# Optimization experiments

Measured on AMD Instinct MI355X. Metric: run time of the kernel, lower is better.

## Reference

```python
import jax, jax.numpy as jnp
import numpy as np

# Fixed problem sizes (equal-sized batch segments, matching setup_inputs)
B, N, M = 4, 4096, 16384          # clouds, coarse pts/cloud, fine pts/cloud
C_IN, C_SKIP, K = 256, 256, 3     # feature dims, knn k
CH = [C_IN + C_SKIP, 512, 256]    # MLP channels
EPS = 1e-16


def setup_inputs() -> dict:
    key = jax.random.key(0)
    ks = jax.random.split(key, 6)
    x = jax.random.normal(ks[0], (B * N, C_IN), jnp.float32)
    pos = jax.random.uniform(ks[1], (B * N, 3), jnp.float32)
    batch = jnp.repeat(jnp.arange(B, dtype=jnp.int64), N)
    x_skip = jax.random.normal(ks[2], (B * M, C_SKIP), jnp.float32)
    pos_skip = jax.random.uniform(ks[3], (B * M, 3), jnp.float32)
    batch_skip = jnp.repeat(jnp.arange(B, dtype=jnp.int64), M)
    W1 = jax.random.normal(ks[4], (CH[0], CH[1]), jnp.float32) / np.sqrt(CH[0]).astype(np.float32)
    b1 = jnp.zeros((CH[1],), jnp.float32)
    W2 = jax.random.normal(ks[5], (CH[1], CH[2]), jnp.float32) / np.sqrt(CH[1]).astype(np.float32)
    b2 = jnp.zeros((CH[2],), jnp.float32)
    return dict(x=x, pos=pos, batch=batch, x_skip=x_skip, pos_skip=pos_skip,
                batch_skip=batch_skip, W1=W1, b1=b1, W2=W2, b2=b2)


def _knn_interpolate(x, pos, pos_skip):
    """torch_geometric.nn.knn_interpolate with equal-sized batch segments."""
    xb = x.reshape(B, N, C_IN)
    ps = pos.reshape(B, N, 3)
    qs = pos_skip.reshape(B, M, 3)
    # squared pairwise distances [B, M, N]
    d2 = (jnp.sum(qs * qs, -1)[:, :, None]
          - 2.0 * jnp.einsum('bmd,bnd->bmn', qs, ps)
          + jnp.sum(ps * ps, -1)[:, None, :])
    neg_d2, idx = jax.lax.top_k(-d2, K)                # k smallest distances, [B,M,K]
    w = 1.0 / jnp.clip(-neg_d2, EPS)                   # inverse squared distance weights
    feats = jax.vmap(lambda f, i: f[i])(xb, idx)       # gather: [B, M, K, C_IN]
    y = jnp.sum(w[..., None] * feats, axis=2) / jnp.sum(w, axis=2)[..., None]
    return y.reshape(B * M, C_IN)


def reference(x, pos, batch, x_skip, pos_skip, batch_skip, W1, b1, W2, b2):
    y = _knn_interpolate(x, pos, pos_skip)
    h = jnp.concatenate([y, x_skip], axis=1)           # [B*M, 512]
    h = jax.nn.relu(h @ W1 + b1)
    h = jax.nn.relu(h @ W2 + b2)
    return h, pos_skip, batch_skip
```

## Files before the change

kernel.cpp:

```cpp
#include <hip/hip_runtime.h>
#include <stdint.h>

#define NB 4
#define NPTS 4096
#define MPTS 16384
#define CIN 256
#define CH0 512
#define CH1 512
#define CH2 256
#define ROWS (NB * MPTS)
#define POS_OUT_OFF (ROWS * CH2)
#define BATCH_OUT_OFF (POS_OUT_OFF + ROWS * 3)
#define CELL_CAP 40
#define QCAP 96

using u16 = unsigned short;
using u32 = unsigned int;
using u64 = unsigned long long;

typedef __bf16 bf16x8 __attribute__((ext_vector_type(8)));
typedef float f32x4 __attribute__((ext_vector_type(4)));

__device__ __forceinline__ u16 f2bf(float f) {
  u32 u = __builtin_bit_cast(u32, f);
  u32 r = u + 0x7fffu + ((u >> 16) & 1u);
  return (u16)(r >> 16);
}

__device__ __forceinline__ u32 flipf(float f) {
  u32 u = __builtin_bit_cast(u32, f);
  return u ^ ((u32)((int)u >> 31) | 0x80000000u);
}
__device__ __forceinline__ float unflipf(u32 f) {
  u32 m = (~(u32)((int)f >> 31)) | 0x80000000u;
  return __builtin_bit_cast(float, f ^ m);
}

__device__ __forceinline__ void ins3(u64 v, u64& k0, u64& k1, u64& k2) {
  u64 a = k0 < v ? v : k0;
  k0 = k0 < v ? k0 : v;
  u64 bb = k1 < a ? a : k1;
  k1 = k1 < a ? k1 : a;
  k2 = k2 < bb ? k2 : bb;
}

__device__ __forceinline__ void merge3(u64 r0, u64 r1, u64 r2,
                                       u64& k0, u64& k1, u64& k2) {
  u64 t = k0 < r0 ? r0 : k0;
  k0 = k0 < r0 ? k0 : r0;
  u64 u = k1 < r1 ? k1 : r1;
  u64 mtu = t < u ? u : t;
  k1 = t < u ? t : u;
  u64 v = k2 < r2 ? k2 : r2;
  k2 = mtu < v ? mtu : v;
}

__device__ __forceinline__ u64 shfl_xor_u64_w8(u64 v, int mask) {
  u32 lo = (u32)v, hi = (u32)(v >> 32);
  lo = (u32)__shfl_xor((int)lo, mask, 8);
  hi = (u32)__shfl_xor((int)hi, mask, 8);
  return ((u64)hi << 32) | lo;
}

__global__ __launch_bounds__(256) void preptail_kernel(
    const float* __restrict__ W1, const float* __restrict__ W2,
    u16* __restrict__ W1s, u16* __restrict__ W2s,
    const float* __restrict__ pos_skip, const int* __restrict__ batch_skip,
    float* __restrict__ out) {
  const int bid = blockIdx.x;
  if (bid < 192) {
    const int t = bid * 256 + threadIdx.x;
    if (t < 32768) {
      const int l = t & 63, ni = (t >> 6) & 3, wd = (t >> 8) & 7, kt = t >> 11;
      const int fr = l & 15, g = l >> 4;
      const int n = wd * 64 + ni * 16 + fr;
      u16 o[8];
#pragma unroll
      for (int j = 0; j < 8; ++j)
        o[j] = f2bf(W1[(kt * 32 + g * 8 + j) * CH1 + n]);
      *(uint4*)(W1s + (size_t)t * 8) = *(const uint4*)o;
    } else {
      const int c = t - 32768;
      const int l = c & 63, ni = (c >> 6) & 1, wd = (c >> 7) & 7, kt = c >> 10;
      const int fr = l & 15, g = l >> 4;
      const int n = wd * 32 + ni * 16 + fr;
      u16 o[8];
#pragma unroll
      for (int j = 0; j < 8; ++j)
        o[j] = f2bf(W2[(kt * 32 + g * 8 + j) * CH2 + n]);
      *(uint4*)(W2s + (size_t)c * 8) = *(const uint4*)o;
    }
  } else {
    const int t = (bid - 192) * 256 + threadIdx.x;
    if (t < ROWS * 3) {
      out[POS_OUT_OFF + t] = pos_skip[t];
    } else {
      int u = t - ROWS * 3;
      out[BATCH_OUT_OFF + u] = (float)batch_skip[u];
    }
  }
}

__global__ __launch_bounds__(256) void bin_kernel(
    const float* __restrict__ pos, float4* __restrict__ pts4,
    u32* __restrict__ cellCnt, int* __restrict__ cellIdx,
    const float* __restrict__ pos_skip, u32* __restrict__ qCnt,
    int* __restrict__ qIdx) {
#pragma clang fp contract(off)
  if (blockIdx.x < 64) {
    const int i = blockIdx.x * 256 + threadIdx.x;
    const float x = pos[i * 3 + 0], y = pos[i * 3 + 1], z = pos[i * 3 + 2];
    pts4[i] = make_float4(x, y, z, (x * x + y * y) + z * z);
    const int b = i >> 12;
    int cx = (int)(x * 8.0f); cx = cx < 0 ? 0 : (cx > 7 ? 7 : cx);
    int cy = (int)(y * 8.0f); cy = cy < 0 ? 0 : (cy > 7 ? 7 : cy);
    int cz = (int)(z * 8.0f); cz = cz < 0 ? 0 : (cz > 7 ? 7 : cz);
    const int c = b * 512 + cz * 64 + cy * 8 + cx;
    const u32 slot = atomicAdd(&cellCnt[c], 1u);
    if (slot < CELL_CAP) cellIdx[c * CELL_CAP + slot] = i;
  } else {
    const int q = (blockIdx.x - 64) * 256 + threadIdx.x;
    const int b = q >> 14;
    const float qx = pos_skip[q * 3 + 0];
    const float qy = pos_skip[q * 3 + 1];
    const float qz = pos_skip[q * 3 + 2];
    int cx = (int)(qx * 8.0f); cx = cx < 0 ? 0 : (cx > 7 ? 7 : cx);
    int cy = (int)(qy * 8.0f); cy = cy < 0 ? 0 : (cy > 7 ? 7 : cy);
    int cz = (int)(qz * 8.0f); cz = cz < 0 ? 0 : (cz > 7 ? 7 : cz);
    const int c = b * 512 + cz * 64 + cy * 8 + cx;
    const u32 slot = atomicAdd(&qCnt[c], 1u);
    if (slot < QCAP) qIdx[c * QCAP + slot] = q;
  }
}

__global__ __launch_bounds__(512) void qperm_kernel(
    const u32* __restrict__ qCnt, const int* __restrict__ qIdx,
    int* __restrict__ qPerm) {
  __shared__ u32 ssc[512];
  const int b = blockIdx.x;
  const int tid = threadIdx.x;
  u32 cnt = qCnt[b * 512 + tid];
  if (cnt > QCAP) cnt = QCAP;
  u32 run = cnt;
  ssc[tid] = run;
  for (int off = 1; off < 512; off <<= 1) {
    __syncthreads();
    u32 t = (tid >= off) ? ssc[tid - off] : 0u;
    __syncthreads();
    run += t;
    ssc[tid] = run;
  }
  const u32 excl = run - cnt;
  const int base = b * MPTS + (int)excl;
  const int src = (b * 512 + tid) * QCAP;
  for (u32 j = 0; j < cnt; ++j)
    qPerm[base + j] = qIdx[src + j];
}

__global__ __launch_bounds__(256) void knn_kernel(
    const float4* __restrict__ pts4, const u32* __restrict__ cellCnt,
    const int* __restrict__ cellIdx, const u32* __restrict__ qCnt,
    const int* __restrict__ qIdx, const float* __restrict__ pos_skip,
    int* __restrict__ idx_out, float* __restrict__ w_out) {
#pragma clang fp contract(off)
  __shared__ float4 scand[27 * CELL_CAP];
  __shared__ int    scgi[27 * CELL_CAP];
  __shared__ u32    scnt[27];
  __shared__ int    sbase[27];
  __shared__ u32    nCand;
  const int tid = threadIdx.x;
  const int b = blockIdx.x >> 9;
  const int cell = blockIdx.x & 511;
  const int cz = cell >> 6, cy = (cell >> 3) & 7, cx = cell & 7;
  const int x0 = cx > 0 ? cx - 1 : 0, x1 = cx < 7 ? cx + 1 : 7;
  const int y0 = cy > 0 ? cy - 1 : 0, y1 = cy < 7 ? cy + 1 : 7;
  const int z0 = cz > 0 ? cz - 1 : 0, z1 = cz < 7 ? cz + 1 : 7;
  const int nx = x1 - x0 + 1, ny = y1 - y0 + 1, nz = z1 - z0 + 1;
  const int ncells = nx * ny * nz;
  if (tid == 0) nCand = 0;
  if (tid < ncells) {
    const int lz = tid / (nx * ny);
    const int rem = tid - lz * nx * ny;
    const int ly = rem / nx;
    const int lx = rem - ly * nx;
    const int cg = b * 512 + (z0 + lz) * 64 + (y0 + ly) * 8 + (x0 + lx);
    u32 cnt = cellCnt[cg];
    scnt[tid] = cnt > CELL_CAP ? CELL_CAP : cnt;
    sbase[tid] = cg * CELL_CAP;
  }
  __syncthreads();
  const int slots = ncells * CELL_CAP;
  for (int s = tid; s < slots; s += 256) {
    const int ci = s / CELL_CAP;
    const int sl = s - ci * CELL_CAP;
    if ((u32)sl < scnt[ci]) {
      const int gi = cellIdx[sbase[ci] + sl];
      const float4 p = pts4[gi];
      const u32 d = atomicAdd(&nCand, 1u);
      scand[d] = p;
      scgi[d] = gi;
    }
  }
  __syncthreads();
  const int nC = (int)nCand;
  u32 nq = qCnt[b * 512 + cell];
  if (nq > QCAP) nq = QCAP;
  const int qbase = (b * 512 + cell) * QCAP;
  const int g = tid >> 3;
  const int sub = tid & 7;

  for (int r0q = 0; r0q < (int)nq; r0q += 32) {
    const int qslot = r0q + g;
    if (qslot < (int)nq) {
      const int q = qIdx[qbase + qslot];
      const float qx = pos_skip[q * 3 + 0];
      const float qy = pos_skip[q * 3 + 1];
      const float qz = pos_skip[q * 3 + 2];
      const float q2 = (qx * qx + qy * qy) + qz * qz;
      u64 k0 = ~0ull, k1 = ~0ull, k2 = ~0ull;
      for (int s = sub; s < nC; s += 8) {
        const float4 p = scand[s];
        const float dot = fmaf(qz, p.z, fmaf(qy, p.y, qx * p.x));
        const float tv = (q2 - 2.0f * dot) + p.w;
        const u64 key = ((u64)flipf(tv) << 32) | (u32)scgi[s];
        ins3(key, k0, k1, k2);
      }
#pragma unroll
      for (int mask = 1; mask < 8; mask <<= 1) {
        const u64 r0 = shfl_xor_u64_w8(k0, mask);
        const u64 r1 = shfl_xor_u64_w8(k1, mask);
        const u64 r2 = shfl_xor_u64_w8(k2, mask);
        merge3(r0, r1, r2, k0, k1, k2);
      }
      float m2tv = unflipf((u32)(k2 >> 32));
      if (!(m2tv <= 0.015625f - 1e-5f)) {
        k0 = k1 = k2 = ~0ull;
        const int ex0 = cx > 1 ? cx - 2 : 0, ex1 = cx < 6 ? cx + 2 : 7;
        const int ey0 = cy > 1 ? cy - 2 : 0, ey1 = cy < 6 ? cy + 2 : 7;
        const int ez0 = cz > 1 ? cz - 2 : 0, ez1 = cz < 6 ? cz + 2 : 7;
        for (int zz = ez0; zz <= ez1; ++zz)
          for (int yy = ey0; yy <= ey1; ++yy)
            for (int xx = ex0; xx <= ex1; ++xx) {
              const int cg = b * 512 + zz * 64 + yy * 8 + xx;
              u32 cnt = cellCnt[cg];
              if (cnt > CELL_CAP) cnt = CELL_CAP;
              const int cb = cg * CELL_CAP;
              for (int s = sub; s < (int)cnt; s += 8) {
                const int gi = cellIdx[cb + s];
                const float4 p = pts4[gi];
                const float dot = fmaf(qz, p.z, fmaf(qy, p.y, qx * p.x));
                const float tv = (q2 - 2.0f * dot) + p.w;
                ins3(((u64)flipf(tv) << 32) | (u32)gi, k0, k1, k2);
              }
            }
#pragma unroll
        for (int mask = 1; mask < 8; mask <<= 1) {
          const u64 r0 = shfl_xor_u64_w8(k0, mask);
          const u64 r1 = shfl_xor_u64_w8(k1, mask);
          const u64 r2 = shfl_xor_u64_w8(k2, mask);
          merge3(r0, r1, r2, k0, k1, k2);
        }
        m2tv = unflipf((u32)(k2 >> 32));
        if (!(m2tv <= 0.0625f - 1e-5f)) {
          k0 = k1 = k2 = ~0ull;
          const int base = b * NPTS;
          for (int i = sub; i < NPTS; i += 8) {
            const int gi = base + i;
            const float4 p = pts4[gi];
            const float dot = fmaf(qz, p.z, fmaf(qy, p.y, qx * p.x));
            const float tv = (q2 - 2.0f * dot) + p.w;
            ins3(((u64)flipf(tv) << 32) | (u32)gi, k0, k1, k2);
          }
#pragma unroll
          for (int mask = 1; mask < 8; mask <<= 1) {
            const u64 r0 = shfl_xor_u64_w8(k0, mask);
            const u64 r1 = shfl_xor_u64_w8(k1, mask);
            const u64 r2 = shfl_xor_u64_w8(k2, mask);
            merge3(r0, r1, r2, k0, k1, k2);
          }
        }
      }
      if (sub == 0) {
        const float t0 = unflipf((u32)(k0 >> 32));
        const float t1 = unflipf((u32)(k1 >> 32));
        const float t2 = unflipf((u32)(k2 >> 32));
        const float w0 = 1.0f / fmaxf(t0, 1e-16f);
        const float w1 = 1.0f / fmaxf(t1, 1e-16f);
        const float w2 = 1.0f / fmaxf(t2, 1e-16f);
        const float wsum = (w0 + w1) + w2;
        const float inv = 1.0f / wsum;
        idx_out[q * 3 + 0] = (int)(u32)k0;
        idx_out[q * 3 + 1] = (int)(u32)k1;
        idx_out[q * 3 + 2] = (int)(u32)k2;
        w_out[q * 3 + 0] = w0 * inv;
        w_out[q * 3 + 1] = w1 * inv;
        w_out[q * 3 + 2] = w2 * inv;
      }
    }
  }
}

__global__ __launch_bounds__(512, 2) void fused_mlp_kernel(
    const float* __restrict__ x, const int* __restrict__ idx,
    const float* __restrict__ w, const float* __restrict__ x_skip,
    const u16* __restrict__ W1s, const float* __restrict__ b1,
    const u16* __restrict__ W2s, const float* __restrict__ b2,
    const int* __restrict__ qPerm, float* __restrict__ out) {
  __shared__ __align__(16) u16 Abuf[64 * 512];
  __shared__ int sPerm[64];
  const int tid = threadIdx.x;
  const int m0 = blockIdx.x * 64;

  if (tid < 64) sPerm[tid] = qPerm[m0 + tid];

  {
    const int row = tid >> 3;
    const int sub = tid & 7;
    const int gr = qPerm[m0 + row];
    u16* rowp = Abuf + row * 512;
    const int rx = row & 7;
    if (sub < 4) {
      const int i0 = idx[gr * 3 + 0], i1 = idx[gr * 3 + 1], i2 = idx[gr * 3 + 2];
      const float w0 = w[gr * 3 + 0], w1 = w[gr * 3 + 1], w2 = w[gr * 3 + 2];
      const float4* p0 = (const float4*)(x + (size_t)i0 * CIN + sub * 64);
      const float4* p1 = (const float4*)(x + (size_t)i1 * CIN + sub * 64);
      const float4* p2 = (const float4*)(x + (size_t)i2 * CIN + sub * 64);
#pragma unroll
      for (int c = 0; c < 8; ++c) {
        const float4 a0 = p0[c * 2], a1 = p1[c * 2], a2 = p2[c * 2];
        const float4 d0 = p0[c * 2 + 1], d1 = p1[c * 2 + 1], d2 = p2[c * 2 + 1];
        u16 o[8];
        o[0] = f2bf(fmaf(w0, a0.x, fmaf(w1, a1.x, w2 * a2.x)));
        o[1] = f2bf(fmaf(w0, a0.y, fmaf(w1, a1.y, w2 * a2.y)));
        o[2] = f2bf(fmaf(w0, a0.z, fmaf(w1, a1.z, w2 * a2.z)));
        o[3] = f2bf(fmaf(w0, a0.w, fmaf(w1, a1.w, w2 * a2.w)));
        o[4] = f2bf(fmaf(w0, d0.x, fmaf(w1, d1.x, w2 * d2.x)));
        o[5] = f2bf(fmaf(w0, d0.y, fmaf(w1, d1.y, w2 * d2.y)));
        o[6] = f2bf(fmaf(w0, d0.z, fmaf(w1, d1.z, w2 * d2.z)));
        o[7] = f2bf(fmaf(w0, d0.w, fmaf(w1, d1.w, w2 * d2.w)));
        const int p = ((c & 3) << 3) | (((2 * sub + (c >> 2)) ^ rx) & 7);
        *(uint4*)(rowp + p * 8) = *(const uint4*)o;
      }
    } else {
      const int ss = sub - 4;
      const float4* ps = (const float4*)(x_skip + (size_t)gr * CIN + ss * 64);
#pragma unroll
      for (int c = 0; c < 8; ++c) {
        const float4 a = ps[c * 2], d = ps[c * 2 + 1];
        u16 o[8];
        o[0] = f2bf(a.x); o[1] = f2bf(a.y); o[2] = f2bf(a.z); o[3] = f2bf(a.w);
        o[4] = f2bf(d.x); o[5] = f2bf(d.y); o[6] = f2bf(d.z); o[7] = f2bf(d.w);
        const int p = 32 | ((c & 3) << 3) | (((2 * ss + (c >> 2)) ^ rx) & 7);
        *(uint4*)(rowp + p * 8) = *(const uint4*)o;
      }
    }
  }
  __syncthreads();

  const int wid = tid >> 6;
  const int lane = tid & 63;
  const int fr = lane & 15;
  const int g = lane >> 4;
  const int frx = fr & 7;

  f32x4 acc[4][4];
#pragma unroll
  for (int mi = 0; mi < 4; mi++)
#pragma unroll
    for (int ni = 0; ni < 4; ni++) acc[mi][ni] = (f32x4){0.f, 0.f, 0.f, 0.f};

  {
    const u16* B1 = W1s + wid * 2048 + lane * 8;
    bf16x8 bf[2][4];
#pragma unroll
    for (int ni = 0; ni < 4; ni++)
      bf[0][ni] = *(const bf16x8*)(B1 + ni * 512);
    for (int kt = 0; kt < 16; ++kt) {
      const int cur = kt & 1;
      if (kt < 15) {
        const u16* nb = B1 + (kt + 1) * 16384;
#pragma unroll
        for (int ni = 0; ni < 4; ni++)
          bf[cur ^ 1][ni] = *(const bf16x8*)(nb + ni * 512);
      }
      bf16x8 af[4];
#pragma unroll
      for (int mi = 0; mi < 4; mi++)
        af[mi] = *(const bf16x8*)&Abuf[(mi * 16 + fr) * 512 +
            ((((kt >> 3) << 5) | (g << 3) | ((kt & 7) ^ frx)) * 8)];
#pragma unroll
      for (int mi = 0; mi < 4; mi++)
#pragma unroll
        for (int ni = 0; ni < 4; ni++)
          acc[mi][ni] = __builtin_amdgcn_mfma_f32_16x16x32_bf16(
              af[mi], bf[cur][ni], acc[mi][ni], 0, 0, 0);
    }
  }
  __syncthreads();

  {
    const int wn = wid * 64;
#pragma unroll
    for (int ni = 0; ni < 4; ni++) {
      const int n = wn + ni * 16 + fr;
      const float bb = b1[n];
      const int vg = n >> 3;
      const int nlow = n & 7;
      const int pb = (vg & 32) | ((vg & 3) << 3) | ((vg >> 2) & 7);
#pragma unroll
      for (int mi = 0; mi < 4; mi++) {
#pragma unroll
        for (int r = 0; r < 4; r++) {
          const int m = mi * 16 + g * 4 + r;
          const float v = fmaxf(acc[mi][ni][r] + bb, 0.f);
          Abuf[m * 512 + (pb ^ (m & 7)) * 8 + nlow] = f2bf(v);
        }
      }
    }
  }
  __syncthreads();

  f32x4 acc2[4][2];
#pragma unroll
  for (int mi = 0; mi < 4; mi++)
#pragma unroll
    for (int ni = 0; ni < 2; ni++) acc2[mi][ni] = (f32x4){0.f, 0.f, 0.f, 0.f};

  {
    const u16* B2 = W2s + wid * 1024 + lane * 8;
    bf16x8 bf[2][2];
#pragma unroll
    for (int ni = 0; ni < 2; ni++)
      bf[0][ni] = *(const bf16x8*)(B2 + ni * 512);
    for (int kt = 0; kt < 16; ++kt) {
      const int cur = kt & 1;
      if (kt < 15) {
        const u16* nb = B2 + (kt + 1) * 8192;
#pragma unroll
        for (int ni = 0; ni < 2; ni++)
          bf[cur ^ 1][ni] = *(const bf16x8*)(nb + ni * 512);
      }
      bf16x8 af[4];
#pragma unroll
      for (int mi = 0; mi < 4; mi++)
        af[mi] = *(const bf16x8*)&Abuf[(mi * 16 + fr) * 512 +
            ((((kt >> 3) << 5) | (g << 3) | ((kt & 7) ^ frx)) * 8)];
#pragma unroll
      for (int mi = 0; mi < 4; mi++)
#pragma unroll
        for (int ni = 0; ni < 2; ni++)
          acc2[mi][ni] = __builtin_amdgcn_mfma_f32_16x16x32_bf16(
              af[mi], bf[cur][ni], acc2[mi][ni], 0, 0, 0);
    }
  }

#pragma unroll
  for (int ni = 0; ni < 2; ni++) {
    const int col = wid * 32 + ni * 16 + fr;
    const float bb = b2[col];
#pragma unroll
    for (int mi = 0; mi < 4; mi++) {
#pragma unroll
      for (int r = 0; r < 4; r++) {
        const int rowg = sPerm[mi * 16 + g * 4 + r];
        out[(size_t)rowg * CH2 + col] = fmaxf(acc2[mi][ni][r] + bb, 0.f);
      }
    }
  }
}

extern "C" void kernel_launch(void* const* d_in, const int* in_sizes, int n_in,
                              void* d_out, int out_size, void* d_ws, size_t ws_size,
                              hipStream_t stream) {
  const float* x        = (const float*)d_in[0];
  const float* pos      = (const float*)d_in[1];
  const float* x_skip   = (const float*)d_in[3];
  const float* pos_skip = (const float*)d_in[4];
  const int*   batch_sk = (const int*)d_in[5];
  const float* W1       = (const float*)d_in[6];
  const float* b1       = (const float*)d_in[7];
  const float* W2       = (const float*)d_in[8];
  const float* b2       = (const float*)d_in[9];
  float* out = (float*)d_out;

  char* ws = (char*)d_ws;
  u16*    W1s     = (u16*)(ws);
  u16*    W2s     = (u16*)(ws + 524288);
  int*    idxb    = (int*)(ws + 786432);
  float*  wb      = (float*)(ws + 1572864);
  float4* pts4    = (float4*)(ws + 2359296);
  u32*    cellCnt = (u32*)(ws + 2621440);
  u32*    qCnt    = (u32*)(ws + 2629632);
  int*    cellIdx = (int*)(ws + 2637824);
  int*    qIdx    = (int*)(ws + 2965504);
  int*    qPerm   = (int*)(ws + 3751936);

  hipMemsetAsync(cellCnt, 0, 16384, stream);
  preptail_kernel<<<dim3(1216), dim3(256), 0, stream>>>(
      W1, W2, W1s, W2s, pos_skip, batch_sk, out);
  bin_kernel<<<dim3(320), dim3(256), 0, stream>>>(
      pos, pts4, cellCnt, cellIdx, pos_skip, qCnt, qIdx);
  qperm_kernel<<<dim3(4), dim3(512), 0, stream>>>(qCnt, qIdx, qPerm);
  knn_kernel<<<dim3(2048), dim3(256), 0, stream>>>(pts4, cellCnt, cellIdx,
                                                   qCnt, qIdx, pos_skip,
                                                   idxb, wb);
  fused_mlp_kernel<<<dim3(1024), dim3(512), 0, stream>>>(
      x, idxb, wb, x_skip, W1s, b1, W2s, b2, qPerm, out);
}
```

Baseline: 267.3 us.

## Fold query permutation into knn launch and double MLP row tile to 128

The separate qperm kernel is removed. Its prefix-scan and permutation now run in four extra blocks appended to the knn launch, which saves one kernel launch. The fused MLP kernel now processes 128 rows per block instead of 64, so each weight fragment loaded from global memory feeds twice as many MFMAs and the block count halves. In exchange, LDS use doubles to 128KB per block and the accumulator registers double, which likely limits occupancy to one block per CU under the (512,2) launch bounds.

```diff
diff --git a/kernel.cpp b/kernel.cpp
--- a/kernel.cpp
+++ b/kernel.cpp
@@ -133,42 +133,44 @@
   }
 }
 
-__global__ __launch_bounds__(512) void qperm_kernel(
-    const u32* __restrict__ qCnt, const int* __restrict__ qIdx,
-    int* __restrict__ qPerm) {
-  __shared__ u32 ssc[512];
-  const int b = blockIdx.x;
-  const int tid = threadIdx.x;
-  u32 cnt = qCnt[b * 512 + tid];
-  if (cnt > QCAP) cnt = QCAP;
-  u32 run = cnt;
-  ssc[tid] = run;
-  for (int off = 1; off < 512; off <<= 1) {
-    __syncthreads();
-    u32 t = (tid >= off) ? ssc[tid - off] : 0u;
-    __syncthreads();
-    run += t;
-    ssc[tid] = run;
-  }
-  const u32 excl = run - cnt;
-  const int base = b * MPTS + (int)excl;
-  const int src = (b * 512 + tid) * QCAP;
-  for (u32 j = 0; j < cnt; ++j)
-    qPerm[base + j] = qIdx[src + j];
-}
-
 __global__ __launch_bounds__(256) void knn_kernel(
     const float4* __restrict__ pts4, const u32* __restrict__ cellCnt,
     const int* __restrict__ cellIdx, const u32* __restrict__ qCnt,
     const int* __restrict__ qIdx, const float* __restrict__ pos_skip,
-    int* __restrict__ idx_out, float* __restrict__ w_out) {
+    int* __restrict__ idx_out, float* __restrict__ w_out,
+    int* __restrict__ qPerm) {
 #pragma clang fp contract(off)
   __shared__ float4 scand[27 * CELL_CAP];
   __shared__ int    scgi[27 * CELL_CAP];
   __shared__ u32    scnt[27];
   __shared__ int    sbase[27];
   __shared__ u32    nCand;
+  __shared__ u32    ssc[256];
   const int tid = threadIdx.x;
+
+  if (blockIdx.x >= 2048) {
+    const int b = blockIdx.x - 2048;
+    u32 c0 = qCnt[b * 512 + 2 * tid];     c0 = c0 > QCAP ? QCAP : c0;
+    u32 c1 = qCnt[b * 512 + 2 * tid + 1]; c1 = c1 > QCAP ? QCAP : c1;
+    const u32 ps = c0 + c1;
+    u32 run = ps;
+    ssc[tid] = run;
+    for (int off = 1; off < 256; off <<= 1) {
+      __syncthreads();
+      u32 t = (tid >= off) ? ssc[tid - off] : 0u;
+      __syncthreads();
+      run += t;
+      ssc[tid] = run;
+    }
+    const u32 excl = run - ps;
+    const int base = b * MPTS + (int)excl;
+    const int s0 = (b * 512 + 2 * tid) * QCAP;
+    const int s1 = (b * 512 + 2 * tid + 1) * QCAP;
+    for (u32 j = 0; j < c0; ++j) qPerm[base + j] = qIdx[s0 + j];
+    for (u32 j = 0; j < c1; ++j) qPerm[base + c0 + j] = qIdx[s1 + j];
+    return;
+  }
+
   const int b = blockIdx.x >> 9;
   const int cell = blockIdx.x & 511;
   const int cz = cell >> 6, cy = (cell >> 3) & 7, cx = cell & 7;
@@ -306,15 +308,16 @@
     const u16* __restrict__ W1s, const float* __restrict__ b1,
     const u16* __restrict__ W2s, const float* __restrict__ b2,
     const int* __restrict__ qPerm, float* __restrict__ out) {
-  __shared__ __align__(16) u16 Abuf[64 * 512];
-  __shared__ int sPerm[64];
+  __shared__ __align__(16) u16 Abuf[128 * 512];
+  __shared__ int sPerm[128];
   const int tid = threadIdx.x;
-  const int m0 = blockIdx.x * 64;
-
-  if (tid < 64) sPerm[tid] = qPerm[m0 + tid];
-
-  {
-    const int row = tid >> 3;
+  const int m0 = blockIdx.x * 128;
+
+  if (tid < 128) sPerm[tid] = qPerm[m0 + tid];
+
+#pragma unroll
+  for (int p = 0; p < 2; ++p) {
+    const int row = p * 64 + (tid >> 3);
     const int sub = tid & 7;
     const int gr = qPerm[m0 + row];
     u16* rowp = Abuf + row * 512;
@@ -338,8 +341,8 @@
         o[5] = f2bf(fmaf(w0, d0.y, fmaf(w1, d1.y, w2 * d2.y)));
         o[6] = f2bf(fmaf(w0, d0.z, fmaf(w1, d1.z, w2 * d2.z)));
         o[7] = f2bf(fmaf(w0, d0.w, fmaf(w1, d1.w, w2 * d2.w)));
-        const int p = ((c & 3) << 3) | (((2 * sub + (c >> 2)) ^ rx) & 7);
-        *(uint4*)(rowp + p * 8) = *(const uint4*)o;
+        const int pp = ((c & 3) << 3) | (((2 * sub + (c >> 2)) ^ rx) & 7);
+        *(uint4*)(rowp + pp * 8) = *(const uint4*)o;
       }
     } else {
       const int ss = sub - 4;
@@ -350,8 +353,8 @@
         u16 o[8];
         o[0] = f2bf(a.x); o[1] = f2bf(a.y); o[2] = f2bf(a.z); o[3] = f2bf(a.w);
         o[4] = f2bf(d.x); o[5] = f2bf(d.y); o[6] = f2bf(d.z); o[7] = f2bf(d.w);
-        const int p = 32 | ((c & 3) << 3) | (((2 * ss + (c >> 2)) ^ rx) & 7);
-        *(uint4*)(rowp + p * 8) = *(const uint4*)o;
+        const int pp = 32 | ((c & 3) << 3) | (((2 * ss + (c >> 2)) ^ rx) & 7);
+        *(uint4*)(rowp + pp * 8) = *(const uint4*)o;
       }
     }
   }
@@ -363,9 +366,9 @@
   const int g = lane >> 4;
   const int frx = fr & 7;
 
-  f32x4 acc[4][4];
-#pragma unroll
-  for (int mi = 0; mi < 4; mi++)
+  f32x4 acc[8][4];
+#pragma unroll
+  for (int mi = 0; mi < 8; mi++)
 #pragma unroll
     for (int ni = 0; ni < 4; ni++) acc[mi][ni] = (f32x4){0.f, 0.f, 0.f, 0.f};
 
@@ -383,17 +386,15 @@
         for (int ni = 0; ni < 4; ni++)
           bf[cur ^ 1][ni] = *(const bf16x8*)(nb + ni * 512);
       }
-      bf16x8 af[4];
-#pragma unroll
-      for (int mi = 0; mi < 4; mi++)
-        af[mi] = *(const bf16x8*)&Abuf[(mi * 16 + fr) * 512 +
+#pragma unroll
+      for (int mi = 0; mi < 8; mi++) {
+        const bf16x8 af = *(const bf16x8*)&Abuf[(mi * 16 + fr) * 512 +
             ((((kt >> 3) << 5) | (g << 3) | ((kt & 7) ^ frx)) * 8)];
-#pragma unroll
-      for (int mi = 0; mi < 4; mi++)
 #pragma unroll
         for (int ni = 0; ni < 4; ni++)
           acc[mi][ni] = __builtin_amdgcn_mfma_f32_16x16x32_bf16(
-              af[mi], bf[cur][ni], acc[mi][ni], 0, 0, 0);
+              af, bf[cur][ni], acc[mi][ni], 0, 0, 0);
+      }
     }
   }
   __syncthreads();
@@ -408,7 +409,7 @@
       const int nlow = n & 7;
       const int pb = (vg & 32) | ((vg & 3) << 3) | ((vg >> 2) & 7);
 #pragma unroll
-      for (int mi = 0; mi < 4; mi++) {
+      for (int mi = 0; mi < 8; mi++) {
 #pragma unroll
         for (int r = 0; r < 4; r++) {
           const int m = mi * 16 + g * 4 + r;
@@ -420,9 +421,9 @@
   }
   __syncthreads();
 
-  f32x4 acc2[4][2];
-#pragma unroll
-  for (int mi = 0; mi < 4; mi++)
+  f32x4 acc2[8][2];
+#pragma unroll
+  for (int mi = 0; mi < 8; mi++)
 #pragma unroll
     for (int ni = 0; ni < 2; ni++) acc2[mi][ni] = (f32x4){0.f, 0.f, 0.f, 0.f};
 
@@ -440,17 +441,15 @@
         for (int ni = 0; ni < 2; ni++)
           bf[cur ^ 1][ni] = *(const bf16x8*)(nb + ni * 512);
       }
-      bf16x8 af[4];
-#pragma unroll
-      for (int mi = 0; mi < 4; mi++)
-        af[mi] = *(const bf16x8*)&Abuf[(mi * 16 + fr) * 512 +
+#pragma unroll
+      for (int mi = 0; mi < 8; mi++) {
+        const bf16x8 af = *(const bf16x8*)&Abuf[(mi * 16 + fr) * 512 +
             ((((kt >> 3) << 5) | (g << 3) | ((kt & 7) ^ frx)) * 8)];
-#pragma unroll
-      for (int mi = 0; mi < 4; mi++)
 #pragma unroll
         for (int ni = 0; ni < 2; ni++)
           acc2[mi][ni] = __builtin_amdgcn_mfma_f32_16x16x32_bf16(
-              af[mi], bf[cur][ni], acc2[mi][ni], 0, 0, 0);
+              af, bf[cur][ni], acc2[mi][ni], 0, 0, 0);
+      }
     }
   }
 
@@ -459,7 +458,7 @@
     const int col = wid * 32 + ni * 16 + fr;
     const float bb = b2[col];
 #pragma unroll
-    for (int mi = 0; mi < 4; mi++) {
+    for (int mi = 0; mi < 8; mi++) {
 #pragma unroll
       for (int r = 0; r < 4; r++) {
         const int rowg = sPerm[mi * 16 + g * 4 + r];
@@ -500,10 +499,9 @@
       W1, W2, W1s, W2s, pos_skip, batch_sk, out);
   bin_kernel<<<dim3(320), dim3(256), 0, stream>>>(
       pos, pts4, cellCnt, cellIdx, pos_skip, qCnt, qIdx);
-  qperm_kernel<<<dim3(4), dim3(512), 0, stream>>>(qCnt, qIdx, qPerm);
-  knn_kernel<<<dim3(2048), dim3(256), 0, stream>>>(pts4, cellCnt, cellIdx,
+  knn_kernel<<<dim3(2052), dim3(256), 0, stream>>>(pts4, cellCnt, cellIdx,
                                                    qCnt, qIdx, pos_skip,
-                                                   idxb, wb);
-  fused_mlp_kernel<<<dim3(1024), dim3(512), 0, stream>>>(
+                                                   idxb, wb, qPerm);
+  fused_mlp_kernel<<<dim3(512), dim3(512), 0, stream>>>(
       x, idxb, wb, x_skip, W1s, b1, W2s, b2, qPerm, out);
 }
```

Measured after the change: 263.7 us. No clear change (-1.3%).

## Fuse binning into prep kernel, fold qperm into knn, defer overflow queries to fixup

Applied to the files above, without the earlier changes.

Merges the weight/tail prep kernel with the point/query binning kernel and folds the query permutation scan into extra blocks of the knn kernel, removing two launches and their serialization gaps. Queries whose 3x3x3 neighbourhood search does not give certified neighbours are no longer handled by 8 lanes inside the knn block. They are appended to an overflow list via an atomic and reprocessed by a new wave-per-query fixup kernel. This removes divergent long tails from knn blocks but adds another launch, a memset and an atomic. The qCnt memset is not visible, and qCnt is now written in the same kernel where cellCnt is zeroed only beforehand.

```diff
diff --git a/kernel.cpp b/kernel.cpp
--- a/kernel.cpp
+++ b/kernel.cpp
@@ -62,11 +62,22 @@
   return ((u64)hi << 32) | lo;
 }
 
-__global__ __launch_bounds__(256) void preptail_kernel(
+__device__ __forceinline__ u64 shfl_xor_u64_w64(u64 v, int mask) {
+  u32 lo = (u32)v, hi = (u32)(v >> 32);
+  lo = (u32)__shfl_xor((int)lo, mask, 64);
+  hi = (u32)__shfl_xor((int)hi, mask, 64);
+  return ((u64)hi << 32) | lo;
+}
+
+__global__ __launch_bounds__(256) void ptbin_kernel(
     const float* __restrict__ W1, const float* __restrict__ W2,
     u16* __restrict__ W1s, u16* __restrict__ W2s,
     const float* __restrict__ pos_skip, const int* __restrict__ batch_skip,
-    float* __restrict__ out) {
+    float* __restrict__ out, const float* __restrict__ pos,
+    float4* __restrict__ pts4, u32* __restrict__ cellCnt,
+    int* __restrict__ cellIdx, u32* __restrict__ qCnt,
+    int* __restrict__ qIdx) {
+#pragma clang fp contract(off)
   const int bid = blockIdx.x;
   if (bid < 192) {
     const int t = bid * 256 + threadIdx.x;
@@ -90,7 +101,7 @@
         o[j] = f2bf(W2[(kt * 32 + g * 8 + j) * CH2 + n]);
       *(uint4*)(W2s + (size_t)c * 8) = *(const uint4*)o;
     }
-  } else {
+  } else if (bid < 1216) {
     const int t = (bid - 192) * 256 + threadIdx.x;
     if (t < ROWS * 3) {
       out[POS_OUT_OFF + t] = pos_skip[t];
@@ -98,17 +109,8 @@
       int u = t - ROWS * 3;
       out[BATCH_OUT_OFF + u] = (float)batch_skip[u];
     }
-  }
-}
-
-__global__ __launch_bounds__(256) void bin_kernel(
-    const float* __restrict__ pos, float4* __restrict__ pts4,
-    u32* __restrict__ cellCnt, int* __restrict__ cellIdx,
-    const float* __restrict__ pos_skip, u32* __restrict__ qCnt,
-    int* __restrict__ qIdx) {
-#pragma clang fp contract(off)
-  if (blockIdx.x < 64) {
-    const int i = blockIdx.x * 256 + threadIdx.x;
+  } else if (bid < 1280) {
+    const int i = (bid - 1216) * 256 + threadIdx.x;
     const float x = pos[i * 3 + 0], y = pos[i * 3 + 1], z = pos[i * 3 + 2];
     pts4[i] = make_float4(x, y, z, (x * x + y * y) + z * z);
     const int b = i >> 12;
@@ -119,7 +121,7 @@
     const u32 slot = atomicAdd(&cellCnt[c], 1u);
     if (slot < CELL_CAP) cellIdx[c * CELL_CAP + slot] = i;
   } else {
-    const int q = (blockIdx.x - 64) * 256 + threadIdx.x;
+    const int q = (bid - 1280) * 256 + threadIdx.x;
     const int b = q >> 14;
     const float qx = pos_skip[q * 3 + 0];
     const float qy = pos_skip[q * 3 + 1];
@@ -133,42 +135,45 @@
   }
 }
 
-__global__ __launch_bounds__(512) void qperm_kernel(
-    const u32* __restrict__ qCnt, const int* __restrict__ qIdx,
-    int* __restrict__ qPerm) {
-  __shared__ u32 ssc[512];
-  const int b = blockIdx.x;
-  const int tid = threadIdx.x;
-  u32 cnt = qCnt[b * 512 + tid];
-  if (cnt > QCAP) cnt = QCAP;
-  u32 run = cnt;
-  ssc[tid] = run;
-  for (int off = 1; off < 512; off <<= 1) {
-    __syncthreads();
-    u32 t = (tid >= off) ? ssc[tid - off] : 0u;
-    __syncthreads();
-    run += t;
-    ssc[tid] = run;
-  }
-  const u32 excl = run - cnt;
-  const int base = b * MPTS + (int)excl;
-  const int src = (b * 512 + tid) * QCAP;
-  for (u32 j = 0; j < cnt; ++j)
-    qPerm[base + j] = qIdx[src + j];
-}
-
 __global__ __launch_bounds__(256) void knn_kernel(
     const float4* __restrict__ pts4, const u32* __restrict__ cellCnt,
     const int* __restrict__ cellIdx, const u32* __restrict__ qCnt,
     const int* __restrict__ qIdx, const float* __restrict__ pos_skip,
-    int* __restrict__ idx_out, float* __restrict__ w_out) {
+    int* __restrict__ idx_out, float* __restrict__ w_out,
+    int* __restrict__ qPerm, u32* __restrict__ ovCnt,
+    int* __restrict__ ovList) {
 #pragma clang fp contract(off)
   __shared__ float4 scand[27 * CELL_CAP];
   __shared__ int    scgi[27 * CELL_CAP];
   __shared__ u32    scnt[27];
   __shared__ int    sbase[27];
   __shared__ u32    nCand;
+  __shared__ u32    ssc[256];
   const int tid = threadIdx.x;
+
+  if (blockIdx.x >= 2048) {
+    const int b = blockIdx.x - 2048;
+    u32 c0 = qCnt[b * 512 + 2 * tid];     c0 = c0 > QCAP ? QCAP : c0;
+    u32 c1 = qCnt[b * 512 + 2 * tid + 1]; c1 = c1 > QCAP ? QCAP : c1;
+    const u32 ps = c0 + c1;
+    u32 run = ps;
+    ssc[tid] = run;
+    for (int off = 1; off < 256; off <<= 1) {
+      __syncthreads();
+      u32 t = (tid >= off) ? ssc[tid - off] : 0u;
+      __syncthreads();
+      run += t;
+      ssc[tid] = run;
+    }
+    const u32 excl = run - ps;
+    const int base = b * MPTS + (int)excl;
+    const int s0 = (b * 512 + 2 * tid) * QCAP;
+    const int s1 = (b * 512 + 2 * tid + 1) * QCAP;
+    for (u32 j = 0; j < c0; ++j) qPerm[base + j] = qIdx[s0 + j];
+    for (u32 j = 0; j < c1; ++j) qPerm[base + c0 + j] = qIdx[s1 + j];
+    return;
+  }
+
   const int b = blockIdx.x >> 9;
   const int cell = blockIdx.x & 511;
   const int cz = cell >> 6, cy = (cell >> 3) & 7, cx = cell & 7;
@@ -232,70 +237,116 @@
         const u64 r2 = shfl_xor_u64_w8(k2, mask);
         merge3(r0, r1, r2, k0, k1, k2);
       }
-      float m2tv = unflipf((u32)(k2 >> 32));
-      if (!(m2tv <= 0.015625f - 1e-5f)) {
-        k0 = k1 = k2 = ~0ull;
-        const int ex0 = cx > 1 ? cx - 2 : 0, ex1 = cx < 6 ? cx + 2 : 7;
-        const int ey0 = cy > 1 ? cy - 2 : 0, ey1 = cy < 6 ? cy + 2 : 7;
-        const int ez0 = cz > 1 ? cz - 2 : 0, ez1 = cz < 6 ? cz + 2 : 7;
-        for (int zz = ez0; zz <= ez1; ++zz)
-          for (int yy = ey0; yy <= ey1; ++yy)
-            for (int xx = ex0; xx <= ex1; ++xx) {
-              const int cg = b * 512 + zz * 64 + yy * 8 + xx;
-              u32 cnt = cellCnt[cg];
-              if (cnt > CELL_CAP) cnt = CELL_CAP;
-              const int cb = cg * CELL_CAP;
-              for (int s = sub; s < (int)cnt; s += 8) {
-                const int gi = cellIdx[cb + s];
-                const float4 p = pts4[gi];
-                const float dot = fmaf(qz, p.z, fmaf(qy, p.y, qx * p.x));
-                const float tv = (q2 - 2.0f * dot) + p.w;
-                ins3(((u64)flipf(tv) << 32) | (u32)gi, k0, k1, k2);
-              }
-            }
-#pragma unroll
-        for (int mask = 1; mask < 8; mask <<= 1) {
-          const u64 r0 = shfl_xor_u64_w8(k0, mask);
-          const u64 r1 = shfl_xor_u64_w8(k1, mask);
-          const u64 r2 = shfl_xor_u64_w8(k2, mask);
-          merge3(r0, r1, r2, k0, k1, k2);
+      const float m2tv = unflipf((u32)(k2 >> 32));
+      if (m2tv <= 0.015625f - 1e-5f) {
+        if (sub == 0) {
+          const float t0 = unflipf((u32)(k0 >> 32));
+          const float t1 = unflipf((u32)(k1 >> 32));
+          const float t2 = unflipf((u32)(k2 >> 32));
+          const float w0 = 1.0f / fmaxf(t0, 1e-16f);
+          const float w1 = 1.0f / fmaxf(t1, 1e-16f);
+          const float w2 = 1.0f / fmaxf(t2, 1e-16f);
+          const float wsum = (w0 + w1) + w2;
+          const float inv = 1.0f / wsum;
+          idx_out[q * 3 + 0] = (int)(u32)k0;
+          idx_out[q * 3 + 1] = (int)(u32)k1;
+          idx_out[q * 3 + 2] = (int)(u32)k2;
+          w_out[q * 3 + 0] = w0 * inv;
+          w_out[q * 3 + 1] = w1 * inv;
+          w_out[q * 3 + 2] = w2 * inv;
         }
-        m2tv = unflipf((u32)(k2 >> 32));
-        if (!(m2tv <= 0.0625f - 1e-5f)) {
-          k0 = k1 = k2 = ~0ull;
-          const int base = b * NPTS;
-          for (int i = sub; i < NPTS; i += 8) {
-            const int gi = base + i;
-            const float4 p = pts4[gi];
-            const float dot = fmaf(qz, p.z, fmaf(qy, p.y, qx * p.x));
-            const float tv = (q2 - 2.0f * dot) + p.w;
-            ins3(((u64)flipf(tv) << 32) | (u32)gi, k0, k1, k2);
-          }
-#pragma unroll
-          for (int mask = 1; mask < 8; mask <<= 1) {
-            const u64 r0 = shfl_xor_u64_w8(k0, mask);
-            const u64 r1 = shfl_xor_u64_w8(k1, mask);
-            const u64 r2 = shfl_xor_u64_w8(k2, mask);
-            merge3(r0, r1, r2, k0, k1, k2);
-          }
-        }
-      }
-      if (sub == 0) {
-        const float t0 = unflipf((u32)(k0 >> 32));
-        const float t1 = unflipf((u32)(k1 >> 32));
-        const float t2 = unflipf((u32)(k2 >> 32));
-        const float w0 = 1.0f / fmaxf(t0, 1e-16f);
-        const float w1 = 1.0f / fmaxf(t1, 1e-16f);
-        const float w2 = 1.0f / fmaxf(t2, 1e-16f);
-        const float wsum = (w0 + w1) + w2;
-        const float inv = 1.0f / wsum;
-        idx_out[q * 3 + 0] = (int)(u32)k0;
-        idx_out[q * 3 + 1] = (int)(u32)k1;
-        idx_out[q * 3 + 2] = (int)(u32)k2;
-        w_out[q * 3 + 0] = w0 * inv;
-        w_out[q * 3 + 1] = w1 * inv;
-        w_out[q * 3 + 2] = w2 * inv;
-      }
+      } else if (sub == 0) {
+        const u32 slot = atomicAdd(ovCnt, 1u);
+        ovList[slot] = q;
+      }
+    }
+  }
+}
+
+__global__ __launch_bounds__(256) void fixup_kernel(
+    const float4* __restrict__ pts4, const u32* __restrict__ cellCnt,
+    const int* __restrict__ cellIdx, const float* __restrict__ pos_skip,
+    const u32* __restrict__ ovCnt, const int* __restrict__ ovList,
+    int* __restrict__ idx_out, float* __restrict__ w_out) {
+#pragma clang fp contract(off)
+  const int tid = threadIdx.x;
+  const int lane = tid & 63;
+  const int wv = tid >> 6;
+  const int nOv = (int)*ovCnt;
+  for (int i = blockIdx.x * 4 + wv; i < nOv; i += gridDim.x * 4) {
+    const int q = ovList[i];
+    const int b = q >> 14;
+    const float qx = pos_skip[q * 3 + 0];
+    const float qy = pos_skip[q * 3 + 1];
+    const float qz = pos_skip[q * 3 + 2];
+    const float q2 = (qx * qx + qy * qy) + qz * qz;
+    int cx = (int)(qx * 8.0f); cx = cx < 0 ? 0 : (cx > 7 ? 7 : cx);
+    int cy = (int)(qy * 8.0f); cy = cy < 0 ? 0 : (cy > 7 ? 7 : cy);
+    int cz = (int)(qz * 8.0f); cz = cz < 0 ? 0 : (cz > 7 ? 7 : cz);
+    const int ex0 = cx > 1 ? cx - 2 : 0, ex1 = cx < 6 ? cx + 2 : 7;
+    const int ey0 = cy > 1 ? cy - 2 : 0, ey1 = cy < 6 ? cy + 2 : 7;
+    const int ez0 = cz > 1 ? cz - 2 : 0, ez1 = cz < 6 ? cz + 2 : 7;
+    const int nx = ex1 - ex0 + 1, ny = ey1 - ey0 + 1, nzc = ez1 - ez0 + 1;
+    const int ncells = nx * ny * nzc;
+    u64 k0 = ~0ull, k1 = ~0ull, k2 = ~0ull;
+    for (int ci = lane; ci < ncells; ci += 64) {
+      const int lz = ci / (nx * ny);
+      const int rem = ci - lz * nx * ny;
+      const int ly = rem / nx;
+      const int lx = rem - ly * nx;
+      const int cg = b * 512 + (ez0 + lz) * 64 + (ey0 + ly) * 8 + (ex0 + lx);
+      u32 cnt = cellCnt[cg];
+      if (cnt > CELL_CAP) cnt = CELL_CAP;
+      const int cb = cg * CELL_CAP;
+      for (u32 s = 0; s < cnt; ++s) {
+        const int gi = cellIdx[cb + s];
+        const float4 p = pts4[gi];
+        const float dot = fmaf(qz, p.z, fmaf(qy, p.y, qx * p.x));
+        const float tv = (q2 - 2.0f * dot) + p.w;
+        ins3(((u64)flipf(tv) << 32) | (u32)gi, k0, k1, k2);
+      }
+    }
+#pragma unroll
+    for (int mask = 1; mask < 64; mask <<= 1) {
+      const u64 r0 = shfl_xor_u64_w64(k0, mask);
+      const u64 r1 = shfl_xor_u64_w64(k1, mask);
+      const u64 r2 = shfl_xor_u64_w64(k2, mask);
+      merge3(r0, r1, r2, k0, k1, k2);
+    }
+    float m2tv = unflipf((u32)(k2 >> 32));
+    if (!(m2tv <= 0.0625f - 1e-5f)) {
+      k0 = k1 = k2 = ~0ull;
+      const int base = b * NPTS;
+      for (int j = lane; j < NPTS; j += 64) {
+        const int gi = base + j;
+        const float4 p = pts4[gi];
+        const float dot = fmaf(qz, p.z, fmaf(qy, p.y, qx * p.x));
+        const float tv = (q2 - 2.0f * dot) + p.w;
+        ins3(((u64)flipf(tv) << 32) | (u32)gi, k0, k1, k2);
+      }
+#pragma unroll
+      for (int mask = 1; mask < 64; mask <<= 1) {
+        const u64 r0 = shfl_xor_u64_w64(k0, mask);
+        const u64 r1 = shfl_xor_u64_w64(k1, mask);
+        const u64 r2 = shfl_xor_u64_w64(k2, mask);
+        merge3(r0, r1, r2, k0, k1, k2);
+      }
+    }
+    if (lane == 0) {
+      const float t0 = unflipf((u32)(k0 >> 32));
+      const float t1 = unflipf((u32)(k1 >> 32));
+      const float t2 = unflipf((u32)(k2 >> 32));
+      const float w0 = 1.0f / fmaxf(t0, 1e-16f);
+      const float w1 = 1.0f / fmaxf(t1, 1e-16f);
+      const float w2 = 1.0f / fmaxf(t2, 1e-16f);
+      const float wsum = (w0 + w1) + w2;
+      const float inv = 1.0f / wsum;
+      idx_out[q * 3 + 0] = (int)(u32)k0;
+      idx_out[q * 3 + 1] = (int)(u32)k1;
+      idx_out[q * 3 + 2] = (int)(u32)k2;
+      w_out[q * 3 + 0] = w0 * inv;
+      w_out[q * 3 + 1] = w1 * inv;
+      w_out[q * 3 + 2] = w2 * inv;
     }
   }
 }
@@ -338,8 +389,8 @@
         o[5] = f2bf(fmaf(w0, d0.y, fmaf(w1, d1.y, w2 * d2.y)));
         o[6] = f2bf(fmaf(w0, d0.z, fmaf(w1, d1.z, w2 * d2.z)));
         o[7] = f2bf(fmaf(w0, d0.w, fmaf(w1, d1.w, w2 * d2.w)));
-        const int p = ((c & 3) << 3) | (((2 * sub + (c >> 2)) ^ rx) & 7);
-        *(uint4*)(rowp + p * 8) = *(const uint4*)o;
+        const int pp = ((c & 3) << 3) | (((2 * sub + (c >> 2)) ^ rx) & 7);
+        *(uint4*)(rowp + pp * 8) = *(const uint4*)o;
       }
     } else {
       const int ss = sub - 4;
@@ -350,8 +401,8 @@
         u16 o[8];
         o[0] = f2bf(a.x); o[1] = f2bf(a.y); o[2] = f2bf(a.z); o[3] = f2bf(a.w);
         o[4] = f2bf(d.x); o[5] = f2bf(d.y); o[6] = f2bf(d.z); o[7] = f2bf(d.w);
-        const int p = 32 | ((c & 3) << 3) | (((2 * ss + (c >> 2)) ^ rx) & 7);
-        *(uint4*)(rowp + p * 8) = *(const uint4*)o;
+        const int pp = 32 | ((c & 3) << 3) | (((2 * ss + (c >> 2)) ^ rx) & 7);
+        *(uint4*)(rowp + pp * 8) = *(const uint4*)o;
       }
     }
   }
@@ -494,16 +545,21 @@
   int*    cellIdx = (int*)(ws + 2637824);
   int*    qIdx    = (int*)(ws + 2965504);
   int*    qPerm   = (int*)(ws + 3751936);
+  u32*    ovCnt   = (u32*)(ws + 4014080);
+  int*    ovList  = (int*)(ws + 4014336);
 
   hipMemsetAsync(cellCnt, 0, 16384, stream);
-  preptail_kernel<<<dim3(1216), dim3(256), 0, stream>>>(
-      W1, W2, W1s, W2s, pos_skip, batch_sk, out);
-  bin_kernel<<<dim3(320), dim3(256), 0, stream>>>(
-      pos, pts4, cellCnt, cellIdx, pos_skip, qCnt, qIdx);
-  qperm_kernel<<<dim3(4), dim3(512), 0, stream>>>(qCnt, qIdx, qPerm);
-  knn_kernel<<<dim3(2048), dim3(256), 0, stream>>>(pts4, cellCnt, cellIdx,
+  hipMemsetAsync(ovCnt, 0, 4, stream);
+  ptbin_kernel<<<dim3(1536), dim3(256), 0, stream>>>(
+      W1, W2, W1s, W2s, pos_skip, batch_sk, out, pos, pts4,
+      cellCnt, cellIdx, qCnt, qIdx);
+  knn_kernel<<<dim3(2052), dim3(256), 0, stream>>>(pts4, cellCnt, cellIdx,
                                                    qCnt, qIdx, pos_skip,
-                                                   idxb, wb);
+                                                   idxb, wb, qPerm,
+                                                   ovCnt, ovList);
+  fixup_kernel<<<dim3(256), dim3(256), 0, stream>>>(pts4, cellCnt, cellIdx,
+                                                    pos_skip, ovCnt, ovList,
+                                                    idxb, wb);
   fused_mlp_kernel<<<dim3(1024), dim3(512), 0, stream>>>(
       x, idxb, wb, x_skip, W1s, b1, W2s, b2, qPerm, out);
 }
```

New measurement: 264.6 us. No clear change (-1.0%).
